# Optimization experiments

Hardware: AMD Instinct MI355X
Metric: run time of the kernel (lower is better)

Reference implementation:

```python
import jax, jax.numpy as jnp
import numpy as np

ND, NC = 100000, 20000
E_DD, E_DC, E_CD = 1600000, 800000, 800000
DDIM, CDIM, H, B = 256, 512, 128, 100000


def _lin_init(k, out_d, in_d):
    kw, kb = jax.random.split(k)
    s = 1.0 / np.sqrt(in_d)
    return (jax.random.uniform(kw, (out_d, in_d), jnp.float32, -s, s),
            jax.random.uniform(kb, (out_d,), jnp.float32, -s, s))


def setup_inputs() -> dict:
    key = jax.random.key(0)
    ks = jax.random.split(key, 32)
    inp = {
        'x_drug': jax.random.normal(ks[0], (ND, DDIM), jnp.float32),
        'x_cell': jax.random.normal(ks[1], (NC, CDIM), jnp.float32),
        'ei_dd_src': jax.random.randint(ks[2], (E_DD,), 0, ND),
        'ei_dd_dst': jax.random.randint(ks[3], (E_DD,), 0, ND),
        'ei_dc_src': jax.random.randint(ks[4], (E_DC,), 0, ND),
        'ei_dc_dst': jax.random.randint(ks[5], (E_DC,), 0, NC),
        'ei_cd_src': jax.random.randint(ks[6], (E_CD,), 0, NC),
        'ei_cd_dst': jax.random.randint(ks[7], (E_CD,), 0, ND),
        'q_da': jax.random.randint(ks[8], (B,), 0, ND),
        'q_db': jax.random.randint(ks[9], (B,), 0, ND),
        'q_c': jax.random.randint(ks[10], (B,), 0, NC),
    }
    # input projections
    inp['wd'], inp['bd'] = _lin_init(ks[11], H, DDIM)
    inp['wc'], inp['bc'] = _lin_init(ks[12], H, CDIM)
    # per-edge-type SAGEConv params: lin_l (W+b, on aggregated neighbors), lin_r (W only, on root)
    i = 13
    for name in ['dd1', 'cd1', 'dc1', 'dd2', 'cd2', 'dc2']:
        wl, bl = _lin_init(ks[i], H, H)
        wr, _ = _lin_init(ks[i + 1], H, H)
        inp[name + '_wl'], inp[name + '_bl'], inp[name + '_wr'] = wl, bl, wr
        i += 2
    # MLP head
    inp['m1_w'], inp['m1_b'] = _lin_init(ks[i], H, 3 * H)
    inp['m2_w'], inp['m2_b'] = _lin_init(ks[i + 1], 1, H)
    return inp


def _sage(x_src, x_dst, src, dst, wl, bl, wr):
    # SAGEConv: mean-aggregate neighbor (src) features onto dst, then lin_l + lin_r(root)
    n_dst = x_dst.shape[0]
    agg = jax.ops.segment_sum(x_src[src], dst, num_segments=n_dst)  # [n_dst, H]
    cnt = jax.ops.segment_sum(jnp.ones(src.shape, x_src.dtype), dst, num_segments=n_dst)
    mean = agg / jnp.maximum(cnt, 1.0)[:, None]
    return mean @ wl.T + bl + x_dst @ wr.T


def reference(x_drug, x_cell, wd, bd, wc, bc,
              dd1_wl, dd1_bl, dd1_wr, cd1_wl, cd1_bl, cd1_wr, dc1_wl, dc1_bl, dc1_wr,
              dd2_wl, dd2_bl, dd2_wr, cd2_wl, cd2_bl, cd2_wr, dc2_wl, dc2_bl, dc2_wr,
              m1_w, m1_b, m2_w, m2_b,
              ei_dd_src, ei_dd_dst, ei_dc_src, ei_dc_dst, ei_cd_src, ei_cd_dst,
              q_da, q_db, q_c):
    xd = x_drug @ wd.T + bd  # [ND, H]
    xc = x_cell @ wc.T + bc  # [NC, H]
    # layer 1 (to_hetero: sum contributions per dst node type, then relu)
    hd = jax.nn.relu(_sage(xd, xd, ei_dd_src, ei_dd_dst, dd1_wl, dd1_bl, dd1_wr)
                     + _sage(xc, xd, ei_cd_src, ei_cd_dst, cd1_wl, cd1_bl, cd1_wr))
    hc = jax.nn.relu(_sage(xd, xc, ei_dc_src, ei_dc_dst, dc1_wl, dc1_bl, dc1_wr))
    # layer 2 (no activation)
    od = (_sage(hd, hd, ei_dd_src, ei_dd_dst, dd2_wl, dd2_bl, dd2_wr)
          + _sage(hc, hd, ei_cd_src, ei_cd_dst, cd2_wl, cd2_bl, cd2_wr))
    oc = _sage(hd, hc, ei_dc_src, ei_dc_dst, dc2_wl, dc2_bl, dc2_wr)
    combined = jnp.concatenate([od[q_da], od[q_db], oc[q_c]], axis=-1)  # [B, 3H]
    h = jax.nn.relu(combined @ m1_w.T + m1_b)  # dropout is eval-mode identity
    return (h @ m2_w.T + m2_b)[:, 0]
```

## Files before the change

### kernel.cpp

```cpp
#include <hip/hip_runtime.h>
#include <hip/hip_fp16.h>

typedef _Float16 f16;
typedef f16 f16x8 __attribute__((ext_vector_type(8)));
typedef float f32x4 __attribute__((ext_vector_type(4)));

#define NDRUG 100000
#define NCELL 20000
#define EDD   1600000
#define EDC   800000
#define ECD   800000
#define NQ    100000
#define ETOT  (EDD + ECD + EDC)
#define NNODE 220000

#define NBD 782
#define NBC 313
#define NBTOT (NBD + NBC)
#define ECHUNK 8192
#define NBLK ((ETOT + ECHUNK - 1) / ECHUNK)
#define BCAP 8192
#define LCAP 6144

__device__ inline int bucket_of(int rdst) { return rdst < 200000 ? (rdst >> 8) : NBD + ((rdst - 200000) >> 6); }
__device__ inline int dl_of(int rdst)     { return rdst < 200000 ? (rdst & 255) : ((rdst - 200000) & 63); }


__global__ __launch_bounds__(256) void scatter_k(
    const int* __restrict__ dds, const int* __restrict__ ddd,
    const int* __restrict__ cds, const int* __restrict__ cdd,
    const int* __restrict__ dcs, const int* __restrict__ dcd,
    int* __restrict__ bucket_cur, unsigned* __restrict__ binned)
{
    __shared__ int lh[NBTOT];
    __shared__ int lbase[NBTOT];

    int tid = threadIdx.x;
    for (int i = tid; i < NBTOT; i += 256) lh[i] = 0;
    __syncthreads();

    int base = blockIdx.x * ECHUNK;
    int end = base + ECHUNK; if (end > ETOT) end = ETOT;

    for (int e = base + tid; e < end; e += 256) {
        int rdst;
        if (e < EDD) rdst = ddd[e];
        else if (e < EDD + ECD) rdst = 100000 + cdd[e - EDD];
        else rdst = 200000 + dcd[e - EDD - ECD];
        atomicAdd(&lh[bucket_of(rdst)], 1);
    }
    __syncthreads();

    for (int i = tid; i < NBTOT; i += 256) {
        int c = lh[i];
        lbase[i] = c ? atomicAdd(&bucket_cur[i], c) : 0;
        lh[i] = 0;
    }
    __syncthreads();

    for (int e = base + tid; e < end; e += 256) {
        int src, rdst;
        if (e < EDD) { src = dds[e]; rdst = ddd[e]; }
        else if (e < EDD + ECD) { int i2 = e - EDD; src = cds[i2]; rdst = 100000 + cdd[i2]; }
        else { int i2 = e - EDD - ECD; src = dcs[i2]; rdst = 200000 + dcd[i2]; }
        int b = bucket_of(rdst);
        int r = atomicAdd(&lh[b], 1);
        binned[lbase[b] + r] = ((unsigned)dl_of(rdst) << 17) | (unsigned)src;
    }
}


__global__ __launch_bounds__(256) void scan_pbase_k(const int* __restrict__ bucket_cur,
                                                    int* __restrict__ pbase, int* __restrict__ rowptr)
{
    __shared__ int seg[256];
    int tid = threadIdx.x;
    int mine[5], s = 0;
#pragma unroll
    for (int q = 0; q < 5; ++q) {
        int idx = tid * 5 + q;
        int t = 0;
        if (idx < NBTOT) {
            t = bucket_cur[idx] - idx * BCAP;
            t = t < 0 ? 0 : (t > LCAP ? LCAP : t);
        }
        mine[q] = t; s += t;
    }
    seg[tid] = s; __syncthreads();
    for (int o = 1; o < 256; o <<= 1) {
        int v = (tid >= o) ? seg[tid - o] : 0;
        __syncthreads();
        seg[tid] += v;
        __syncthreads();
    }
    int run = seg[tid] - s;
#pragma unroll
    for (int q = 0; q < 5; ++q) {
        int idx = tid * 5 + q;
        if (idx < NBTOT) pbase[idx] = run;
        run += mine[q];
    }
    if (tid == 255) { pbase[NBTOT] = seg[255]; rowptr[NNODE] = seg[255]; }
}


__global__ __launch_bounds__(256) void bucket_build_k(
    const unsigned* __restrict__ binned, const int* __restrict__ bucket_cur, const int* __restrict__ pbase,
    int* __restrict__ rowptr, int* __restrict__ packed)
{
    __shared__ int cnt[256];
    __shared__ int off[256];
    __shared__ int seg[256];
    __shared__ unsigned short lrank[LCAP];
    __shared__ unsigned srec[LCAP];

    int b = blockIdx.x, tid = threadIdx.x;
    int gbase = b * BCAP;
    int n = bucket_cur[b] - gbase;
    n = n < 0 ? 0 : (n > LCAP ? LCAP : n);
    int pb = pbase[b];

    cnt[tid] = 0;
    __syncthreads();
    for (int j = tid; j < n; j += 256) {
        unsigned r = binned[gbase + j];
        lrank[j] = (unsigned short)atomicAdd(&cnt[r >> 17], 1);
    }
    __syncthreads();
    int c = cnt[tid];
    seg[tid] = c; __syncthreads();
    for (int o = 1; o < 256; o <<= 1) {
        int v = (tid >= o) ? seg[tid - o] : 0;
        __syncthreads();
        seg[tid] += v;
        __syncthreads();
    }
    off[tid] = seg[tid] - c;
    __syncthreads();

    if (b < NBD) {
        int rdst = b * 256 + tid;
        if (rdst < 200000) rowptr[rdst] = pb + off[tid];
    } else {
        if (tid < 64) {
            int node = (b - NBD) * 64 + tid;
            if (node < NCELL) rowptr[200000 + node] = pb + off[tid];
        }
    }

    for (int j = tid; j < n; j += 256) {
        unsigned r = binned[gbase + j];
        int p = off[r >> 17] + lrank[j];
        srec[p] = r & 0x1FFFF;
    }
    __syncthreads();

    for (int p = tid; p < n; p += 256) packed[pb + p] = (int)srec[p];
}


__global__ __launch_bounds__(256) void cvt16_k(const float* __restrict__ xd, f16* __restrict__ xd16,
                                               const float* __restrict__ xc, f16* __restrict__ xc16)
{
    const long TD = (long)NDRUG * 256 / 8;
    const long TC = (long)NCELL * 512 / 8;
    long stride = (long)gridDim.x * 256;
    for (long t = (long)blockIdx.x * 256 + threadIdx.x; t < TD + TC; t += stride) {
        const float* src; f16* dst;
        long p;
        if (t < TD) { src = xd; dst = xd16; p = t; }
        else        { src = xc; dst = xc16; p = t - TD; }
        const float4* sp = (const float4*)(src + p * 8);
        float4 u = sp[0], v = sp[1];
        f16x8 h;
        h[0] = (f16)u.x; h[1] = (f16)u.y; h[2] = (f16)u.z; h[3] = (f16)u.w;
        h[4] = (f16)v.x; h[5] = (f16)v.y; h[6] = (f16)v.z; h[7] = (f16)v.w;
        *(f16x8*)(dst + p * 8) = h;
    }
}


__device__ inline void addv(float* acc, uint4 v)
{
    const __half2* h = (const __half2*)&v;
#pragma unroll
    for (int j = 0; j < 4; ++j) {
        float2 f = __half22float2(h[j]);
        acc[2 * j]     += f.x;
        acc[2 * j + 1] += f.y;
    }
}

__global__ __launch_bounds__(256) void agg_all_k(
    const __half* __restrict__ t_d, const __half* __restrict__ t_c,
    const int* __restrict__ rowptr, const int* __restrict__ packed,
    __half* __restrict__ m_a, __half* __restrict__ m_b, __half* __restrict__ m_c)
{
    int gid = blockIdx.x * 16 + (threadIdx.x >> 4);
    if (gid >= NNODE) return;
    int g = threadIdx.x & 15;

    const __half* tab; __half* out;
    if (gid < 100000)      { tab = t_d; out = m_a + (size_t)gid * 128; }
    else if (gid < 200000) { tab = t_c; out = m_b + (size_t)(gid - 100000) * 128; }
    else                   { tab = t_d; out = m_c + (size_t)(gid - 200000) * 128; }

    int s = rowptr[gid];
    int n = rowptr[gid + 1] - s;
    const int* list = packed + s;
    const __half* base = tab + (size_t)g * 8;

    float acc[8];
#pragma unroll
    for (int j = 0; j < 8; ++j) acc[j] = 0.f;

    int i = 0;
    for (; i + 3 < n; i += 4) {
        int s0 = list[i], s1 = list[i + 1], s2 = list[i + 2], s3 = list[i + 3];
        uint4 v0 = *(const uint4*)(base + (size_t)s0 * 128);
        uint4 v1 = *(const uint4*)(base + (size_t)s1 * 128);
        uint4 v2 = *(const uint4*)(base + (size_t)s2 * 128);
        uint4 v3 = *(const uint4*)(base + (size_t)s3 * 128);
        addv(acc, v0); addv(acc, v1); addv(acc, v2); addv(acc, v3);
    }
    for (; i < n; ++i) {
        uint4 v = *(const uint4*)(base + (size_t)list[i] * 128);
        addv(acc, v);
    }

    float inv = 1.f / fmaxf((float)n, 1.f);
    __half h[8];
#pragma unroll
    for (int j = 0; j < 8; ++j) h[j] = __float2half(acc[j] * inv);
    *(uint4*)(out + g * 8) = *(uint4*)h;
}


__global__ __launch_bounds__(256) void prep_k(
    const float* __restrict__ wd,     const float* __restrict__ wc,     const float* __restrict__ m1w,
    const float* __restrict__ dd1_wl, const float* __restrict__ cd1_wl, const float* __restrict__ dc1_wl,
    const float* __restrict__ dc1_wr, const float* __restrict__ dd1_wr, const float* __restrict__ cd1_wr,
    const float* __restrict__ dd1_bl, const float* __restrict__ cd1_bl,
    const float* __restrict__ dd2_wl, const float* __restrict__ cd2_wl, const float* __restrict__ dc2_wl,
    const float* __restrict__ dc2_wr, const float* __restrict__ dd2_wr, const float* __restrict__ cd2_wr,
    const float* __restrict__ dd2_bl, const float* __restrict__ cd2_bl,
    f16* __restrict__ wd16, f16* __restrict__ wc16, f16* __restrict__ m1w16,
    f16* __restrict__ dd1_wl16, f16* __restrict__ cd1_wl16, f16* __restrict__ dc1_wl16,
    f16* __restrict__ dc1_wr16, f16* __restrict__ wr1s16,
    f16* __restrict__ dd2_wl16, f16* __restrict__ cd2_wl16, f16* __restrict__ dc2_wl16,
    f16* __restrict__ dc2_wr16, f16* __restrict__ wr2s16,
    float* __restrict__ bsum1, float* __restrict__ bsum2,
    int* __restrict__ bucket_cur)
{
    int i = blockIdx.x * 256 + threadIdx.x;
    if (i < 128 * 256) wd16[i] = (f16)wd[i];
    if (i < 128 * 512) wc16[i] = (f16)wc[i];
    if (i < 128 * 384) m1w16[i] = (f16)m1w[i];
    if (i < 128 * 128) {
        dd1_wl16[i] = (f16)dd1_wl[i];
        cd1_wl16[i] = (f16)cd1_wl[i];
        dc1_wl16[i] = (f16)dc1_wl[i];
        dc1_wr16[i] = (f16)dc1_wr[i];
        wr1s16[i]   = (f16)(dd1_wr[i] + cd1_wr[i]);
        dd2_wl16[i] = (f16)dd2_wl[i];
        cd2_wl16[i] = (f16)cd2_wl[i];
        dc2_wl16[i] = (f16)dc2_wl[i];
        dc2_wr16[i] = (f16)dc2_wr[i];
        wr2s16[i]   = (f16)(dd2_wr[i] + cd2_wr[i]);
    }
    if (i < 128) {
        bsum1[i] = dd1_bl[i] + cd1_bl[i];
        bsum2[i] = dd2_bl[i] + cd2_bl[i];
    }
    if (i < NBTOT) bucket_cur[i] = i * BCAP;
}


template<typename AT, int MODE>
__global__ __launch_bounds__(256) void mgemm_k(
    const AT* A00, const int* I00, const f16* W00, int K00, int S00,
    const AT* A01, const int* I01, const f16* W01, int K01, int S01,
    const AT* A02, const int* I02, const f16* W02, int K02, int S02,
    const float* bias0, f16* Ch0, int M0,
    const AT* A10, const int* I10, const f16* W10, int K10, int S10,
    const AT* A11, const int* I11, const f16* W11, int K11, int S11,
    const AT* A12, const int* I12, const f16* W12, int K12, int S12,
    const float* bias1, f16* Ch1, int M1,
    int split,
    const float* m2w, const float* m2b, float* Cf)
{
    __shared__ f16 As[128][72];
    __shared__ f16 Ws[128][72];

    const int tid = threadIdx.x;
    const int w  = tid >> 6;
    const int l  = tid & 63;
    const int lc = l & 15;
    const int lq = l >> 4;
    const int sr = tid >> 1;
    const int sk = (tid & 1) * 32;

    const bool j1 = (int)blockIdx.x >= split;
    const int mb = ((int)blockIdx.x - (j1 ? split : 0)) * 128;
    const AT*  Aseg[3] = { j1 ? A10 : A00, j1 ? A11 : A01, j1 ? A12 : A02 };
    const int* Iseg[3] = { j1 ? I10 : I00, j1 ? I11 : I01, j1 ? I12 : I02 };
    const f16* Wseg[3] = { j1 ? W10 : W00, j1 ? W11 : W01, j1 ? W12 : W02 };
    const int  Kseg[3] = { j1 ? K10 : K00, j1 ? K11 : K01, j1 ? K12 : K02 };
    const int  Sseg[3] = { j1 ? S10 : S00, j1 ? S11 : S01, j1 ? S12 : S02 };
    const float* bias = j1 ? bias1 : bias0;
    f16* Ch = j1 ? Ch1 : Ch0;
    const int M = j1 ? M1 : M0;

    f32x4 acc[2][8];
#pragma unroll
    for (int mi = 0; mi < 2; ++mi)
#pragma unroll
        for (int j = 0; j < 8; ++j) acc[mi][j] = (f32x4){0.f, 0.f, 0.f, 0.f};

    for (int s = 0; s < 3; ++s) {
        const AT* A = Aseg[s];
        if (!A) continue;
        const int* idx = Iseg[s];
        const f16* W = Wseg[s];
        const int K = Kseg[s], S = Sseg[s];

        int m = mb + sr; if (m >= M) m = M - 1;
        const AT*  arow = A + (size_t)(idx ? idx[m] : m) * (size_t)K;
        const f16* wrow = W + (size_t)sr * (size_t)S;

        for (int kt = 0; kt < K; kt += 64) {
            if constexpr (sizeof(AT) == 2) {
                const uint4* ap = (const uint4*)(arow + kt + sk);
                uint4 a0 = ap[0], a1 = ap[1], a2 = ap[2], a3 = ap[3];
                *(uint4*)&As[sr][sk]      = a0;
                *(uint4*)&As[sr][sk + 8]  = a1;
                *(uint4*)&As[sr][sk + 16] = a2;
                *(uint4*)&As[sr][sk + 24] = a3;
            } else {
                const float4* ap = (const float4*)(arow + kt + sk);
#pragma unroll
                for (int i = 0; i < 4; ++i) {
                    float4 u = ap[2 * i], v = ap[2 * i + 1];
                    f16x8 h;
                    h[0] = (f16)u.x; h[1] = (f16)u.y; h[2] = (f16)u.z; h[3] = (f16)u.w;
                    h[4] = (f16)v.x; h[5] = (f16)v.y; h[6] = (f16)v.z; h[7] = (f16)v.w;
                    *(f16x8*)&As[sr][sk + 8 * i] = h;
                }
            }
            {
                const uint4* wp = (const uint4*)(wrow + kt + sk);
                uint4 w0 = wp[0], w1 = wp[1], w2 = wp[2], w3 = wp[3];
                *(uint4*)&Ws[sr][sk]      = w0;
                *(uint4*)&Ws[sr][sk + 8]  = w1;
                *(uint4*)&Ws[sr][sk + 16] = w2;
                *(uint4*)&Ws[sr][sk + 24] = w3;
            }
            __syncthreads();

#pragma unroll
            for (int ks = 0; ks < 64; ks += 32) {
                f16x8 a0 = *(const f16x8*)&As[32 * w + lc][ks + 8 * lq];
                f16x8 a1 = *(const f16x8*)&As[32 * w + 16 + lc][ks + 8 * lq];
#pragma unroll
                for (int j = 0; j < 8; ++j) {
                    f16x8 b = *(const f16x8*)&Ws[16 * j + lc][ks + 8 * lq];
                    acc[0][j] = __builtin_amdgcn_mfma_f32_16x16x32_f16(a0, b, acc[0][j], 0, 0, 0);
                    acc[1][j] = __builtin_amdgcn_mfma_f32_16x16x32_f16(a1, b, acc[1][j], 0, 0, 0);
                }
            }
            __syncthreads();
        }
    }

    if (MODE == 2) {
        float part[2][4];
#pragma unroll
        for (int mi = 0; mi < 2; ++mi)
#pragma unroll
            for (int r = 0; r < 4; ++r) part[mi][r] = 0.f;
#pragma unroll
        for (int j = 0; j < 8; ++j) {
            float bj = bias[16 * j + lc];
            float wv = m2w[16 * j + lc];
#pragma unroll
            for (int mi = 0; mi < 2; ++mi)
#pragma unroll
                for (int r = 0; r < 4; ++r) {
                    float v = acc[mi][j][r] + bj;
                    v = v > 0.f ? v : 0.f;
                    part[mi][r] = fmaf(v, wv, part[mi][r]);
                }
        }
#pragma unroll
        for (int mi = 0; mi < 2; ++mi)
#pragma unroll
            for (int r = 0; r < 4; ++r) {
                float p = part[mi][r];
#pragma unroll
                for (int o = 1; o < 16; o <<= 1) p += __shfl_xor(p, o, 16);
                if (lc == 0) {
                    int row = mb + 32 * w + 16 * mi + 4 * lq + r;
                    if (row < M) Cf[row] = p + m2b[0];
                }
            }
    } else {
#pragma unroll
        for (int j = 0; j < 8; ++j) {
            float bj = bias[16 * j + lc];
#pragma unroll
            for (int mi = 0; mi < 2; ++mi)
#pragma unroll
                for (int r = 0; r < 4; ++r) {
                    float v = acc[mi][j][r] + bj;
                    if (MODE == 1) v = v > 0.f ? v : 0.f;
                    int row = mb + 32 * w + 16 * mi + 4 * lq + r;
                    if (row < M) Ch[(size_t)row * 128 + 16 * j + lc] = (f16)v;
                }
        }
    }
}


extern "C" void kernel_launch(void* const* d_in, const int* in_sizes, int n_in,
                              void* d_out, int out_size, void* d_ws, size_t ws_size,
                              hipStream_t stream)
{
    const float* x_drug = (const float*)d_in[0];
    const float* x_cell = (const float*)d_in[1];
    const int* ei_dd_src = (const int*)d_in[2];
    const int* ei_dd_dst = (const int*)d_in[3];
    const int* ei_dc_src = (const int*)d_in[4];
    const int* ei_dc_dst = (const int*)d_in[5];
    const int* ei_cd_src = (const int*)d_in[6];
    const int* ei_cd_dst = (const int*)d_in[7];
    const int* q_da = (const int*)d_in[8];
    const int* q_db = (const int*)d_in[9];
    const int* q_c  = (const int*)d_in[10];
    const float* wd = (const float*)d_in[11];
    const float* bd = (const float*)d_in[12];
    const float* wc = (const float*)d_in[13];
    const float* bc = (const float*)d_in[14];
    const float* dd1_wl = (const float*)d_in[15]; const float* dd1_bl = (const float*)d_in[16]; const float* dd1_wr = (const float*)d_in[17];
    const float* cd1_wl = (const float*)d_in[18]; const float* cd1_bl = (const float*)d_in[19]; const float* cd1_wr = (const float*)d_in[20];
    const float* dc1_wl = (const float*)d_in[21]; const float* dc1_bl = (const float*)d_in[22]; const float* dc1_wr = (const float*)d_in[23];
    const float* dd2_wl = (const float*)d_in[24]; const float* dd2_bl = (const float*)d_in[25]; const float* dd2_wr = (const float*)d_in[26];
    const float* cd2_wl = (const float*)d_in[27]; const float* cd2_bl = (const float*)d_in[28]; const float* cd2_wr = (const float*)d_in[29];
    const float* dc2_wl = (const float*)d_in[30]; const float* dc2_bl = (const float*)d_in[31]; const float* dc2_wr = (const float*)d_in[32];
    const float* m1_w = (const float*)d_in[33]; const float* m1_b = (const float*)d_in[34];
    const float* m2_w = (const float*)d_in[35]; const float* m2_b = (const float*)d_in[36];
    float* out = (float*)d_out;

    char* wsp = (char*)d_ws;
    size_t off = 0;
    auto alloc = [&](size_t bytes) -> void* {
        void* p = wsp + off;
        off += (bytes + 255) & ~(size_t)255;
        return p;
    };

    f16* xd32_16 = (f16*)alloc((size_t)NDRUG * 256 * 2);
    f16* xc32_16 = (f16*)alloc((size_t)NCELL * 512 * 2);

    __half* xd_h     = (__half*)alloc((size_t)NDRUG * 128 * 2);
    __half* xc_h     = (__half*)alloc((size_t)NCELL * 128 * 2);
    __half* hd_h     = (__half*)alloc((size_t)NDRUG * 128 * 2);
    __half* hc_h     = (__half*)alloc((size_t)NCELL * 128 * 2);
    __half* mean_a_h = (__half*)alloc((size_t)NDRUG * 128 * 2);
    __half* mean_b_h = (__half*)alloc((size_t)NDRUG * 128 * 2);
    __half* mean_c_h = (__half*)alloc((size_t)NCELL * 128 * 2);
    __half* od_h     = (__half*)alloc((size_t)NDRUG * 128 * 2);
    __half* oc_h     = (__half*)alloc((size_t)NCELL * 128 * 2);

    f16* wd16     = (f16*)alloc(128 * 256 * 2);
    f16* wc16     = (f16*)alloc(128 * 512 * 2);
    f16* m1w16    = (f16*)alloc(128 * 384 * 2);
    f16* dd1_wl16 = (f16*)alloc(128 * 128 * 2);
    f16* cd1_wl16 = (f16*)alloc(128 * 128 * 2);
    f16* dc1_wl16 = (f16*)alloc(128 * 128 * 2);
    f16* dc1_wr16 = (f16*)alloc(128 * 128 * 2);
    f16* wr1s16   = (f16*)alloc(128 * 128 * 2);
    f16* dd2_wl16 = (f16*)alloc(128 * 128 * 2);
    f16* cd2_wl16 = (f16*)alloc(128 * 128 * 2);
    f16* dc2_wl16 = (f16*)alloc(128 * 128 * 2);
    f16* dc2_wr16 = (f16*)alloc(128 * 128 * 2);
    f16* wr2s16   = (f16*)alloc(128 * 128 * 2);
    float* bsum1  = (float*)alloc(128 * 4);
    float* bsum2  = (float*)alloc(128 * 4);

    int* bucket_cur  = (int*)alloc((size_t)NBTOT * 4);
    int* pbase       = (int*)alloc((size_t)(NBTOT + 1) * 4);
    int* rowptr      = (int*)alloc((size_t)(NNODE + 1) * 4);
    int* packed      = (int*)alloc((size_t)ETOT * 4);
    unsigned* binned = (unsigned*)alloc((size_t)NBTOT * BCAP * 4);

    prep_k<<<256, 256, 0, stream>>>(
        wd, wc, m1_w,
        dd1_wl, cd1_wl, dc1_wl, dc1_wr, dd1_wr, cd1_wr, dd1_bl, cd1_bl,
        dd2_wl, cd2_wl, dc2_wl, dc2_wr, dd2_wr, cd2_wr, dd2_bl, cd2_bl,
        wd16, wc16, m1w16,
        dd1_wl16, cd1_wl16, dc1_wl16, dc1_wr16, wr1s16,
        dd2_wl16, cd2_wl16, dc2_wl16, dc2_wr16, wr2s16,
        bsum1, bsum2, bucket_cur);

    cvt16_k<<<4096, 256, 0, stream>>>(x_drug, xd32_16, x_cell, xc32_16);

    scatter_k<<<NBLK, 256, 0, stream>>>(ei_dd_src, ei_dd_dst, ei_cd_src, ei_cd_dst,
                                        ei_dc_src, ei_dc_dst, bucket_cur, binned);
    scan_pbase_k<<<1, 256, 0, stream>>>(bucket_cur, pbase, rowptr);
    bucket_build_k<<<NBTOT, 256, 0, stream>>>(binned, bucket_cur, pbase, rowptr, packed);

    const f16*   fnull = nullptr;
    const float* f32null = nullptr;
    const int*   inull = nullptr;
    const int GD = (NDRUG + 127) / 128;
    const int GC = (NCELL + 127) / 128;
    const int GQ = (NQ + 127) / 128;

    mgemm_k<f16, 0><<<GD + GC, 256, 0, stream>>>(
        xc32_16, inull, wc16, 512, 512,
        fnull, inull, fnull, 0, 0,
        fnull, inull, fnull, 0, 0,
        bc, (f16*)xc_h, NCELL,
        xd32_16, inull, wd16, 256, 256,
        fnull, inull, fnull, 0, 0,
        fnull, inull, fnull, 0, 0,
        bd, (f16*)xd_h, NDRUG,
        GC, f32null, f32null, nullptr);

    const int AGG_GRID = (NNODE + 15) / 16;

    agg_all_k<<<AGG_GRID, 256, 0, stream>>>(xd_h, xc_h, rowptr, packed,
                                            mean_a_h, mean_b_h, mean_c_h);

    mgemm_k<f16, 1><<<GD + GC, 256, 0, stream>>>(
        (const f16*)mean_c_h, inull, dc1_wl16, 128, 128,
        (const f16*)xc_h,     inull, dc1_wr16, 128, 128,
        fnull,                inull, fnull,    0, 0,
        dc1_bl, (f16*)hc_h, NCELL,
        (const f16*)mean_a_h, inull, dd1_wl16, 128, 128,
        (const f16*)mean_b_h, inull, cd1_wl16, 128, 128,
        (const f16*)xd_h,     inull, wr1s16,   128, 128,
        bsum1, (f16*)hd_h, NDRUG,
        GC, f32null, f32null, nullptr);

    agg_all_k<<<AGG_GRID, 256, 0, stream>>>(hd_h, hc_h, rowptr, packed,
                                            mean_a_h, mean_b_h, mean_c_h);

    mgemm_k<f16, 0><<<GD + GC, 256, 0, stream>>>(
        (const f16*)mean_c_h, inull, dc2_wl16, 128, 128,
        (const f16*)hc_h,     inull, dc2_wr16, 128, 128,
        fnull,                inull, fnull,    0, 0,
        dc2_bl, (f16*)oc_h, NCELL,
        (const f16*)mean_a_h, inull, dd2_wl16, 128, 128,
        (const f16*)mean_b_h, inull, cd2_wl16, 128, 128,
        (const f16*)hd_h,     inull, wr2s16,   128, 128,
        bsum2, (f16*)od_h, NDRUG,
        GC, f32null, f32null, nullptr);

    mgemm_k<f16, 2><<<GQ, 256, 0, stream>>>(
        (const f16*)od_h, q_da, m1w16,       128, 384,
        (const f16*)od_h, q_db, m1w16 + 128, 128, 384,
        (const f16*)oc_h, q_c,  m1w16 + 256, 128, 384,
        m1_b, nullptr, NQ,
        fnull, inull, fnull, 0, 0,
        fnull, inull, fnull, 0, 0,
        fnull, inull, fnull, 0, 0,
        f32null, nullptr, 0,
        GQ, m2_w, m2_b, out);
}
```

Measured before the change: 482.2 us.

## Merge graph-build stages with conversion and projection kernels, drop compacted CSR

The fp32-to-fp16 conversion now runs as extra blocks inside the edge scatter kernel. The bucket sort and the input projection GEMM share one launch through a shared-memory union. The prefix scan over buckets and the separate packed array are removed: sorted edges are written back in place into the padded binned buffer, and aggregation reads a per-node count array instead of rowptr[i+1]. This cuts three launches, one global scan and one copy of the edge list, at the cost of larger shared-memory footprints and more heterogeneous blocks per kernel.

Measured after the change: 467.3 us. -3.1%, faster.

```diff
diff --git a/kernel.cpp b/kernel.cpp
--- a/kernel.cpp
+++ b/kernel.cpp
@@ -21,161 +21,276 @@
 #define NBLK ((ETOT + ECHUNK - 1) / ECHUNK)
 #define BCAP 8192
 #define LCAP 6144
+#define CVTG 2048
+#define GC_PROJ 157
+#define GD_PROJ 782
 
 __device__ inline int bucket_of(int rdst) { return rdst < 200000 ? (rdst >> 8) : NBD + ((rdst - 200000) >> 6); }
 __device__ inline int dl_of(int rdst)     { return rdst < 200000 ? (rdst & 255) : ((rdst - 200000) & 63); }
 
 
-__global__ __launch_bounds__(256) void scatter_k(
+struct GemmSh { f16 As[128][72]; f16 Ws[128][72]; };
+struct BktSh {
+    int cnt[256]; int off[256]; int seg[256];
+    unsigned short lrank[LCAP];
+    unsigned srec[LCAP];
+};
+union ShU { GemmSh g; BktSh b; };
+
+
+template<typename AT, int MODE>
+__device__ __forceinline__ void gemm_core(
+    f16 (*As)[72], f16 (*Ws)[72], int mb,
+    const AT* A0, const int* I0, const f16* W0, int K0, int S0,
+    const AT* A1, const int* I1, const f16* W1, int K1, int S1,
+    const AT* A2, const int* I2, const f16* W2, int K2, int S2,
+    const float* bias, f16* Ch, int M,
+    const float* m2w, const float* m2b, float* Cf)
+{
+    const int tid = threadIdx.x;
+    const int w  = tid >> 6;
+    const int l  = tid & 63;
+    const int lc = l & 15;
+    const int lq = l >> 4;
+    const int sr = tid >> 1;
+    const int sk = (tid & 1) * 32;
+
+    f32x4 acc[2][8];
+#pragma unroll
+    for (int mi = 0; mi < 2; ++mi)
+#pragma unroll
+        for (int j = 0; j < 8; ++j) acc[mi][j] = (f32x4){0.f, 0.f, 0.f, 0.f};
+
+    const AT*  Aseg[3] = {A0, A1, A2};
+    const int* Iseg[3] = {I0, I1, I2};
+    const f16* Wseg[3] = {W0, W1, W2};
+    const int  Kseg[3] = {K0, K1, K2};
+    const int  Sseg[3] = {S0, S1, S2};
+
+    for (int s = 0; s < 3; ++s) {
+        const AT* A = Aseg[s];
+        if (!A) continue;
+        const int* idx = Iseg[s];
+        const f16* W = Wseg[s];
+        const int K = Kseg[s], S = Sseg[s];
+
+        int m = mb + sr; if (m >= M) m = M - 1;
+        const AT*  arow = A + (size_t)(idx ? idx[m] : m) * (size_t)K;
+        const f16* wrow = W + (size_t)sr * (size_t)S;
+
+        for (int kt = 0; kt < K; kt += 64) {
+            {
+                const uint4* ap = (const uint4*)(arow + kt + sk);
+                uint4 a0 = ap[0], a1 = ap[1], a2 = ap[2], a3 = ap[3];
+                *(uint4*)&As[sr][sk]      = a0;
+                *(uint4*)&As[sr][sk + 8]  = a1;
+                *(uint4*)&As[sr][sk + 16] = a2;
+                *(uint4*)&As[sr][sk + 24] = a3;
+            }
+            {
+                const uint4* wp = (const uint4*)(wrow + kt + sk);
+                uint4 w0 = wp[0], w1 = wp[1], w2 = wp[2], w3 = wp[3];
+                *(uint4*)&Ws[sr][sk]      = w0;
+                *(uint4*)&Ws[sr][sk + 8]  = w1;
+                *(uint4*)&Ws[sr][sk + 16] = w2;
+                *(uint4*)&Ws[sr][sk + 24] = w3;
+            }
+            __syncthreads();
+
+#pragma unroll
+            for (int ks = 0; ks < 64; ks += 32) {
+                f16x8 a0 = *(const f16x8*)&As[32 * w + lc][ks + 8 * lq];
+                f16x8 a1 = *(const f16x8*)&As[32 * w + 16 + lc][ks + 8 * lq];
+#pragma unroll
+                for (int j = 0; j < 8; ++j) {
+                    f16x8 b = *(const f16x8*)&Ws[16 * j + lc][ks + 8 * lq];
+                    acc[0][j] = __builtin_amdgcn_mfma_f32_16x16x32_f16(a0, b, acc[0][j], 0, 0, 0);
+                    acc[1][j] = __builtin_amdgcn_mfma_f32_16x16x32_f16(a1, b, acc[1][j], 0, 0, 0);
+                }
+            }
+            __syncthreads();
+        }
+    }
+
+    if (MODE == 2) {
+        float part[2][4];
+#pragma unroll
+        for (int mi = 0; mi < 2; ++mi)
+#pragma unroll
+            for (int r = 0; r < 4; ++r) part[mi][r] = 0.f;
+#pragma unroll
+        for (int j = 0; j < 8; ++j) {
+            float bj = bias[16 * j + lc];
+            float wv = m2w[16 * j + lc];
+#pragma unroll
+            for (int mi = 0; mi < 2; ++mi)
+#pragma unroll
+                for (int r = 0; r < 4; ++r) {
+                    float v = acc[mi][j][r] + bj;
+                    v = v > 0.f ? v : 0.f;
+                    part[mi][r] = fmaf(v, wv, part[mi][r]);
+                }
+        }
+#pragma unroll
+        for (int mi = 0; mi < 2; ++mi)
+#pragma unroll
+            for (int r = 0; r < 4; ++r) {
+                float p = part[mi][r];
+#pragma unroll
+                for (int o = 1; o < 16; o <<= 1) p += __shfl_xor(p, o, 16);
+                if (lc == 0) {
+                    int row = mb + 32 * w + 16 * mi + 4 * lq + r;
+                    if (row < M) Cf[row] = p + m2b[0];
+                }
+            }
+    } else {
+#pragma unroll
+        for (int j = 0; j < 8; ++j) {
+            float bj = bias[16 * j + lc];
+#pragma unroll
+            for (int mi = 0; mi < 2; ++mi)
+#pragma unroll
+                for (int r = 0; r < 4; ++r) {
+                    float v = acc[mi][j][r] + bj;
+                    if (MODE == 1) v = v > 0.f ? v : 0.f;
+                    int row = mb + 32 * w + 16 * mi + 4 * lq + r;
+                    if (row < M) Ch[(size_t)row * 128 + 16 * j + lc] = (f16)v;
+                }
+        }
+    }
+}
+
+
+__global__ __launch_bounds__(256) void scatter_cvt_k(
     const int* __restrict__ dds, const int* __restrict__ ddd,
     const int* __restrict__ cds, const int* __restrict__ cdd,
     const int* __restrict__ dcs, const int* __restrict__ dcd,
-    int* __restrict__ bucket_cur, unsigned* __restrict__ binned)
+    int* __restrict__ bucket_cur, unsigned* __restrict__ binned,
+    const float* __restrict__ xd, f16* __restrict__ xd16,
+    const float* __restrict__ xc, f16* __restrict__ xc16)
 {
     __shared__ int lh[NBTOT];
     __shared__ int lbase[NBTOT];
-
     int tid = threadIdx.x;
-    for (int i = tid; i < NBTOT; i += 256) lh[i] = 0;
-    __syncthreads();
-
-    int base = blockIdx.x * ECHUNK;
-    int end = base + ECHUNK; if (end > ETOT) end = ETOT;
-
-    for (int e = base + tid; e < end; e += 256) {
-        int rdst;
-        if (e < EDD) rdst = ddd[e];
-        else if (e < EDD + ECD) rdst = 100000 + cdd[e - EDD];
-        else rdst = 200000 + dcd[e - EDD - ECD];
-        atomicAdd(&lh[bucket_of(rdst)], 1);
-    }
-    __syncthreads();
-
-    for (int i = tid; i < NBTOT; i += 256) {
-        int c = lh[i];
-        lbase[i] = c ? atomicAdd(&bucket_cur[i], c) : 0;
-        lh[i] = 0;
-    }
-    __syncthreads();
-
-    for (int e = base + tid; e < end; e += 256) {
-        int src, rdst;
-        if (e < EDD) { src = dds[e]; rdst = ddd[e]; }
-        else if (e < EDD + ECD) { int i2 = e - EDD; src = cds[i2]; rdst = 100000 + cdd[i2]; }
-        else { int i2 = e - EDD - ECD; src = dcs[i2]; rdst = 200000 + dcd[i2]; }
-        int b = bucket_of(rdst);
-        int r = atomicAdd(&lh[b], 1);
-        binned[lbase[b] + r] = ((unsigned)dl_of(rdst) << 17) | (unsigned)src;
-    }
-}
-
-
-__global__ __launch_bounds__(256) void scan_pbase_k(const int* __restrict__ bucket_cur,
-                                                    int* __restrict__ pbase, int* __restrict__ rowptr)
-{
-    __shared__ int seg[256];
+
+    if ((int)blockIdx.x < NBLK) {
+        for (int i = tid; i < NBTOT; i += 256) lh[i] = 0;
+        __syncthreads();
+
+        int base = blockIdx.x * ECHUNK;
+        int end = base + ECHUNK; if (end > ETOT) end = ETOT;
+
+        for (int e = base + tid; e < end; e += 256) {
+            int rdst;
+            if (e < EDD) rdst = ddd[e];
+            else if (e < EDD + ECD) rdst = 100000 + cdd[e - EDD];
+            else rdst = 200000 + dcd[e - EDD - ECD];
+            atomicAdd(&lh[bucket_of(rdst)], 1);
+        }
+        __syncthreads();
+
+        for (int i = tid; i < NBTOT; i += 256) {
+            int c = lh[i];
+            lbase[i] = c ? atomicAdd(&bucket_cur[i], c) : 0;
+            lh[i] = 0;
+        }
+        __syncthreads();
+
+        for (int e = base + tid; e < end; e += 256) {
+            int src, rdst;
+            if (e < EDD) { src = dds[e]; rdst = ddd[e]; }
+            else if (e < EDD + ECD) { int i2 = e - EDD; src = cds[i2]; rdst = 100000 + cdd[i2]; }
+            else { int i2 = e - EDD - ECD; src = dcs[i2]; rdst = 200000 + dcd[i2]; }
+            int b = bucket_of(rdst);
+            int r = atomicAdd(&lh[b], 1);
+            binned[lbase[b] + r] = ((unsigned)dl_of(rdst) << 17) | (unsigned)src;
+        }
+    } else {
+        const long TD = (long)NDRUG * 256 / 8;
+        const long TC = (long)NCELL * 512 / 8;
+        long stride = (long)CVTG * 256;
+        for (long t = (long)((int)blockIdx.x - NBLK) * 256 + tid; t < TD + TC; t += stride) {
+            const float* src; f16* dst; long p;
+            if (t < TD) { src = xd; dst = xd16; p = t; }
+            else        { src = xc; dst = xc16; p = t - TD; }
+            const float4* sp = (const float4*)(src + p * 8);
+            float4 u = sp[0], v = sp[1];
+            f16x8 h;
+            h[0] = (f16)u.x; h[1] = (f16)u.y; h[2] = (f16)u.z; h[3] = (f16)u.w;
+            h[4] = (f16)v.x; h[5] = (f16)v.y; h[6] = (f16)v.z; h[7] = (f16)v.w;
+            *(f16x8*)(dst + p * 8) = h;
+        }
+    }
+}
+
+
+__global__ __launch_bounds__(256) void bucket_proj_k(
+    unsigned* __restrict__ binned, const int* __restrict__ bucket_cur,
+    int* __restrict__ rowptr, int* __restrict__ cnt_arr,
+    const f16* __restrict__ xc32_16, const f16* __restrict__ wc16, const float* __restrict__ bc, f16* __restrict__ xc_h,
+    const f16* __restrict__ xd32_16, const f16* __restrict__ wd16, const float* __restrict__ bd, f16* __restrict__ xd_h)
+{
+    __shared__ ShU sh;
     int tid = threadIdx.x;
-    int mine[5], s = 0;
-#pragma unroll
-    for (int q = 0; q < 5; ++q) {
-        int idx = tid * 5 + q;
-        int t = 0;
-        if (idx < NBTOT) {
-            t = bucket_cur[idx] - idx * BCAP;
-            t = t < 0 ? 0 : (t > LCAP ? LCAP : t);
-        }
-        mine[q] = t; s += t;
-    }
-    seg[tid] = s; __syncthreads();
-    for (int o = 1; o < 256; o <<= 1) {
-        int v = (tid >= o) ? seg[tid - o] : 0;
-        __syncthreads();
-        seg[tid] += v;
-        __syncthreads();
-    }
-    int run = seg[tid] - s;
-#pragma unroll
-    for (int q = 0; q < 5; ++q) {
-        int idx = tid * 5 + q;
-        if (idx < NBTOT) pbase[idx] = run;
-        run += mine[q];
-    }
-    if (tid == 255) { pbase[NBTOT] = seg[255]; rowptr[NNODE] = seg[255]; }
-}
-
-
-__global__ __launch_bounds__(256) void bucket_build_k(
-    const unsigned* __restrict__ binned, const int* __restrict__ bucket_cur, const int* __restrict__ pbase,
-    int* __restrict__ rowptr, int* __restrict__ packed)
-{
-    __shared__ int cnt[256];
-    __shared__ int off[256];
-    __shared__ int seg[256];
-    __shared__ unsigned short lrank[LCAP];
-    __shared__ unsigned srec[LCAP];
-
-    int b = blockIdx.x, tid = threadIdx.x;
-    int gbase = b * BCAP;
-    int n = bucket_cur[b] - gbase;
-    n = n < 0 ? 0 : (n > LCAP ? LCAP : n);
-    int pb = pbase[b];
-
-    cnt[tid] = 0;
-    __syncthreads();
-    for (int j = tid; j < n; j += 256) {
-        unsigned r = binned[gbase + j];
-        lrank[j] = (unsigned short)atomicAdd(&cnt[r >> 17], 1);
-    }
-    __syncthreads();
-    int c = cnt[tid];
-    seg[tid] = c; __syncthreads();
-    for (int o = 1; o < 256; o <<= 1) {
-        int v = (tid >= o) ? seg[tid - o] : 0;
-        __syncthreads();
-        seg[tid] += v;
-        __syncthreads();
-    }
-    off[tid] = seg[tid] - c;
-    __syncthreads();
-
-    if (b < NBD) {
-        int rdst = b * 256 + tid;
-        if (rdst < 200000) rowptr[rdst] = pb + off[tid];
+
+    if ((int)blockIdx.x < NBTOT) {
+        int b = blockIdx.x;
+        int gbase = b * BCAP;
+        int n = bucket_cur[b] - gbase;
+        n = n < 0 ? 0 : (n > LCAP ? LCAP : n);
+
+        sh.b.cnt[tid] = 0;
+        __syncthreads();
+        for (int j = tid; j < n; j += 256) {
+            unsigned r = binned[gbase + j];
+            sh.b.lrank[j] = (unsigned short)atomicAdd(&sh.b.cnt[r >> 17], 1);
+        }
+        __syncthreads();
+        int c = sh.b.cnt[tid];
+        sh.b.seg[tid] = c; __syncthreads();
+        for (int o = 1; o < 256; o <<= 1) {
+            int v = (tid >= o) ? sh.b.seg[tid - o] : 0;
+            __syncthreads();
+            sh.b.seg[tid] += v;
+            __syncthreads();
+        }
+        sh.b.off[tid] = sh.b.seg[tid] - c;
+        __syncthreads();
+
+        if (b < NBD) {
+            int rdst = b * 256 + tid;
+            if (rdst < 200000) { rowptr[rdst] = gbase + sh.b.off[tid]; cnt_arr[rdst] = c; }
+        } else {
+            if (tid < 64) {
+                int node = (b - NBD) * 64 + tid;
+                if (node < NCELL) { rowptr[200000 + node] = gbase + sh.b.off[tid]; cnt_arr[200000 + node] = c; }
+            }
+        }
+
+        for (int j = tid; j < n; j += 256) {
+            unsigned r = binned[gbase + j];
+            int p = sh.b.off[r >> 17] + sh.b.lrank[j];
+            sh.b.srec[p] = r & 0x1FFFF;
+        }
+        __syncthreads();
+
+        for (int p = tid; p < n; p += 256) binned[gbase + p] = sh.b.srec[p];
     } else {
-        if (tid < 64) {
-            int node = (b - NBD) * 64 + tid;
-            if (node < NCELL) rowptr[200000 + node] = pb + off[tid];
-        }
-    }
-
-    for (int j = tid; j < n; j += 256) {
-        unsigned r = binned[gbase + j];
-        int p = off[r >> 17] + lrank[j];
-        srec[p] = r & 0x1FFFF;
-    }
-    __syncthreads();
-
-    for (int p = tid; p < n; p += 256) packed[pb + p] = (int)srec[p];
-}
-
-
-__global__ __launch_bounds__(256) void cvt16_k(const float* __restrict__ xd, f16* __restrict__ xd16,
-                                               const float* __restrict__ xc, f16* __restrict__ xc16)
-{
-    const long TD = (long)NDRUG * 256 / 8;
-    const long TC = (long)NCELL * 512 / 8;
-    long stride = (long)gridDim.x * 256;
-    for (long t = (long)blockIdx.x * 256 + threadIdx.x; t < TD + TC; t += stride) {
-        const float* src; f16* dst;
-        long p;
-        if (t < TD) { src = xd; dst = xd16; p = t; }
-        else        { src = xc; dst = xc16; p = t - TD; }
-        const float4* sp = (const float4*)(src + p * 8);
-        float4 u = sp[0], v = sp[1];
-        f16x8 h;
-        h[0] = (f16)u.x; h[1] = (f16)u.y; h[2] = (f16)u.z; h[3] = (f16)u.w;
-        h[4] = (f16)v.x; h[5] = (f16)v.y; h[6] = (f16)v.z; h[7] = (f16)v.w;
-        *(f16x8*)(dst + p * 8) = h;
+        int bid = (int)blockIdx.x - NBTOT;
+        const f16* fn = nullptr; const int* in_ = nullptr;
+        if (bid < GC_PROJ) {
+            gemm_core<f16, 0>(sh.g.As, sh.g.Ws, bid * 128,
+                xc32_16, in_, wc16, 512, 512,
+                fn, in_, fn, 0, 0,
+                fn, in_, fn, 0, 0,
+                bc, xc_h, NCELL, nullptr, nullptr, nullptr);
+        } else {
+            gemm_core<f16, 0>(sh.g.As, sh.g.Ws, (bid - GC_PROJ) * 128,
+                xd32_16, in_, wd16, 256, 256,
+                fn, in_, fn, 0, 0,
+                fn, in_, fn, 0, 0,
+                bd, xd_h, NDRUG, nullptr, nullptr, nullptr);
+        }
     }
 }
 
@@ -193,7 +308,8 @@
 
 __global__ __launch_bounds__(256) void agg_all_k(
     const __half* __restrict__ t_d, const __half* __restrict__ t_c,
-    const int* __restrict__ rowptr, const int* __restrict__ packed,
+    const int* __restrict__ rowptr, const int* __restrict__ cnt_arr,
+    const unsigned* __restrict__ packed,
     __half* __restrict__ m_a, __half* __restrict__ m_b, __half* __restrict__ m_c)
 {
     int gid = blockIdx.x * 16 + (threadIdx.x >> 4);
@@ -206,8 +322,8 @@
     else                   { tab = t_d; out = m_c + (size_t)(gid - 200000) * 128; }
 
     int s = rowptr[gid];
-    int n = rowptr[gid + 1] - s;
-    const int* list = packed + s;
+    int n = cnt_arr[gid];
+    const unsigned* list = packed + s;
     const __half* base = tab + (size_t)g * 8;
 
     float acc[8];
@@ -216,7 +332,7 @@
 
     int i = 0;
     for (; i + 3 < n; i += 4) {
-        int s0 = list[i], s1 = list[i + 1], s2 = list[i + 2], s3 = list[i + 3];
+        unsigned s0 = list[i], s1 = list[i + 1], s2 = list[i + 2], s3 = list[i + 3];
         uint4 v0 = *(const uint4*)(base + (size_t)s0 * 128);
         uint4 v1 = *(const uint4*)(base + (size_t)s1 * 128);
         uint4 v2 = *(const uint4*)(base + (size_t)s2 * 128);
@@ -291,133 +407,14 @@
 {
     __shared__ f16 As[128][72];
     __shared__ f16 Ws[128][72];
-
-    const int tid = threadIdx.x;
-    const int w  = tid >> 6;
-    const int l  = tid & 63;
-    const int lc = l & 15;
-    const int lq = l >> 4;
-    const int sr = tid >> 1;
-    const int sk = (tid & 1) * 32;
-
     const bool j1 = (int)blockIdx.x >= split;
     const int mb = ((int)blockIdx.x - (j1 ? split : 0)) * 128;
-    const AT*  Aseg[3] = { j1 ? A10 : A00, j1 ? A11 : A01, j1 ? A12 : A02 };
-    const int* Iseg[3] = { j1 ? I10 : I00, j1 ? I11 : I01, j1 ? I12 : I02 };
-    const f16* Wseg[3] = { j1 ? W10 : W00, j1 ? W11 : W01, j1 ? W12 : W02 };
-    const int  Kseg[3] = { j1 ? K10 : K00, j1 ? K11 : K01, j1 ? K12 : K02 };
-    const int  Sseg[3] = { j1 ? S10 : S00, j1 ? S11 : S01, j1 ? S12 : S02 };
-    const float* bias = j1 ? bias1 : bias0;
-    f16* Ch = j1 ? Ch1 : Ch0;
-    const int M = j1 ? M1 : M0;
-
-    f32x4 acc[2][8];
-#pragma unroll
-    for (int mi = 0; mi < 2; ++mi)
-#pragma unroll
-        for (int j = 0; j < 8; ++j) acc[mi][j] = (f32x4){0.f, 0.f, 0.f, 0.f};
-
-    for (int s = 0; s < 3; ++s) {
-        const AT* A = Aseg[s];
-        if (!A) continue;
-        const int* idx = Iseg[s];
-        const f16* W = Wseg[s];
-        const int K = Kseg[s], S = Sseg[s];
-
-        int m = mb + sr; if (m >= M) m = M - 1;
-        const AT*  arow = A + (size_t)(idx ? idx[m] : m) * (size_t)K;
-        const f16* wrow = W + (size_t)sr * (size_t)S;
-
-        for (int kt = 0; kt < K; kt += 64) {
-            if constexpr (sizeof(AT) == 2) {
-                const uint4* ap = (const uint4*)(arow + kt + sk);
-                uint4 a0 = ap[0], a1 = ap[1], a2 = ap[2], a3 = ap[3];
-                *(uint4*)&As[sr][sk]      = a0;
-                *(uint4*)&As[sr][sk + 8]  = a1;
-                *(uint4*)&As[sr][sk + 16] = a2;
-                *(uint4*)&As[sr][sk + 24] = a3;
-            } else {
-                const float4* ap = (const float4*)(arow + kt + sk);
-#pragma unroll
-                for (int i = 0; i < 4; ++i) {
-                    float4 u = ap[2 * i], v = ap[2 * i + 1];
-                    f16x8 h;
-                    h[0] = (f16)u.x; h[1] = (f16)u.y; h[2] = (f16)u.z; h[3] = (f16)u.w;
-                    h[4] = (f16)v.x; h[5] = (f16)v.y; h[6] = (f16)v.z; h[7] = (f16)v.w;
-                    *(f16x8*)&As[sr][sk + 8 * i] = h;
-                }
-            }
-            {
-                const uint4* wp = (const uint4*)(wrow + kt + sk);
-                uint4 w0 = wp[0], w1 = wp[1], w2 = wp[2], w3 = wp[3];
-                *(uint4*)&Ws[sr][sk]      = w0;
-                *(uint4*)&Ws[sr][sk + 8]  = w1;
-                *(uint4*)&Ws[sr][sk + 16] = w2;
-                *(uint4*)&Ws[sr][sk + 24] = w3;
-            }
-            __syncthreads();
-
-#pragma unroll
-            for (int ks = 0; ks < 64; ks += 32) {
-                f16x8 a0 = *(const f16x8*)&As[32 * w + lc][ks + 8 * lq];
-                f16x8 a1 = *(const f16x8*)&As[32 * w + 16 + lc][ks + 8 * lq];
-#pragma unroll
-                for (int j = 0; j < 8; ++j) {
-                    f16x8 b = *(const f16x8*)&Ws[16 * j + lc][ks + 8 * lq];
-                    acc[0][j] = __builtin_amdgcn_mfma_f32_16x16x32_f16(a0, b, acc[0][j], 0, 0, 0);
-                    acc[1][j] = __builtin_amdgcn_mfma_f32_16x16x32_f16(a1, b, acc[1][j], 0, 0, 0);
-                }
-            }
-            __syncthreads();
-        }
-    }
-
-    if (MODE == 2) {
-        float part[2][4];
-#pragma unroll
-        for (int mi = 0; mi < 2; ++mi)
-#pragma unroll
-            for (int r = 0; r < 4; ++r) part[mi][r] = 0.f;
-#pragma unroll
-        for (int j = 0; j < 8; ++j) {
-            float bj = bias[16 * j + lc];
-            float wv = m2w[16 * j + lc];
-#pragma unroll
-            for (int mi = 0; mi < 2; ++mi)
-#pragma unroll
-                for (int r = 0; r < 4; ++r) {
-                    float v = acc[mi][j][r] + bj;
-                    v = v > 0.f ? v : 0.f;
-                    part[mi][r] = fmaf(v, wv, part[mi][r]);
-                }
-        }
-#pragma unroll
-        for (int mi = 0; mi < 2; ++mi)
-#pragma unroll
-            for (int r = 0; r < 4; ++r) {
-                float p = part[mi][r];
-#pragma unroll
-                for (int o = 1; o < 16; o <<= 1) p += __shfl_xor(p, o, 16);
-                if (lc == 0) {
-                    int row = mb + 32 * w + 16 * mi + 4 * lq + r;
-                    if (row < M) Cf[row] = p + m2b[0];
-                }
-            }
-    } else {
-#pragma unroll
-        for (int j = 0; j < 8; ++j) {
-            float bj = bias[16 * j + lc];
-#pragma unroll
-            for (int mi = 0; mi < 2; ++mi)
-#pragma unroll
-                for (int r = 0; r < 4; ++r) {
-                    float v = acc[mi][j][r] + bj;
-                    if (MODE == 1) v = v > 0.f ? v : 0.f;
-                    int row = mb + 32 * w + 16 * mi + 4 * lq + r;
-                    if (row < M) Ch[(size_t)row * 128 + 16 * j + lc] = (f16)v;
-                }
-        }
-    }
+    if (!j1)
+        gemm_core<AT, MODE>(As, Ws, mb, A00, I00, W00, K00, S00, A01, I01, W01, K01, S01,
+                            A02, I02, W02, K02, S02, bias0, Ch0, M0, m2w, m2b, Cf);
+    else
+        gemm_core<AT, MODE>(As, Ws, mb, A10, I10, W10, K10, S10, A11, I11, W11, K11, S11,
+                            A12, I12, W12, K12, S12, bias1, Ch1, M1, m2w, m2b, Cf);
 }
 
 
@@ -488,9 +485,8 @@
     float* bsum2  = (float*)alloc(128 * 4);
 
     int* bucket_cur  = (int*)alloc((size_t)NBTOT * 4);
-    int* pbase       = (int*)alloc((size_t)(NBTOT + 1) * 4);
-    int* rowptr      = (int*)alloc((size_t)(NNODE + 1) * 4);
-    int* packed      = (int*)alloc((size_t)ETOT * 4);
+    int* rowptr      = (int*)alloc((size_t)NNODE * 4);
+    int* cnt_arr     = (int*)alloc((size_t)NNODE * 4);
     unsigned* binned = (unsigned*)alloc((size_t)NBTOT * BCAP * 4);
 
     prep_k<<<256, 256, 0, stream>>>(
@@ -502,34 +498,25 @@
         dd2_wl16, cd2_wl16, dc2_wl16, dc2_wr16, wr2s16,
         bsum1, bsum2, bucket_cur);
 
-    cvt16_k<<<4096, 256, 0, stream>>>(x_drug, xd32_16, x_cell, xc32_16);
-
-    scatter_k<<<NBLK, 256, 0, stream>>>(ei_dd_src, ei_dd_dst, ei_cd_src, ei_cd_dst,
-                                        ei_dc_src, ei_dc_dst, bucket_cur, binned);
-    scan_pbase_k<<<1, 256, 0, stream>>>(bucket_cur, pbase, rowptr);
-    bucket_build_k<<<NBTOT, 256, 0, stream>>>(binned, bucket_cur, pbase, rowptr, packed);
+    scatter_cvt_k<<<NBLK + CVTG, 256, 0, stream>>>(
+        ei_dd_src, ei_dd_dst, ei_cd_src, ei_cd_dst, ei_dc_src, ei_dc_dst,
+        bucket_cur, binned, x_drug, xd32_16, x_cell, xc32_16);
+
+    bucket_proj_k<<<NBTOT + GC_PROJ + GD_PROJ, 256, 0, stream>>>(
+        binned, bucket_cur, rowptr, cnt_arr,
+        xc32_16, wc16, bc, (f16*)xc_h,
+        xd32_16, wd16, bd, (f16*)xd_h);
 
     const f16*   fnull = nullptr;
     const float* f32null = nullptr;
     const int*   inull = nullptr;
-    const int GD = (NDRUG + 127) / 128;
-    const int GC = (NCELL + 127) / 128;
+    const int GD = GD_PROJ;
+    const int GC = GC_PROJ;
     const int GQ = (NQ + 127) / 128;
 
-    mgemm_k<f16, 0><<<GD + GC, 256, 0, stream>>>(
-        xc32_16, inull, wc16, 512, 512,
-        fnull, inull, fnull, 0, 0,
-        fnull, inull, fnull, 0, 0,
-        bc, (f16*)xc_h, NCELL,
-        xd32_16, inull, wd16, 256, 256,
-        fnull, inull, fnull, 0, 0,
-        fnull, inull, fnull, 0, 0,
-        bd, (f16*)xd_h, NDRUG,
-        GC, f32null, f32null, nullptr);
-
     const int AGG_GRID = (NNODE + 15) / 16;
 
-    agg_all_k<<<AGG_GRID, 256, 0, stream>>>(xd_h, xc_h, rowptr, packed,
+    agg_all_k<<<AGG_GRID, 256, 0, stream>>>(xd_h, xc_h, rowptr, cnt_arr, binned,
                                             mean_a_h, mean_b_h, mean_c_h);
 
     mgemm_k<f16, 1><<<GD + GC, 256, 0, stream>>>(
@@ -543,7 +530,7 @@
         bsum1, (f16*)hd_h, NDRUG,
         GC, f32null, f32null, nullptr);
 
-    agg_all_k<<<AGG_GRID, 256, 0, stream>>>(hd_h, hc_h, rowptr, packed,
+    agg_all_k<<<AGG_GRID, 256, 0, stream>>>(hd_h, hc_h, rowptr, cnt_arr, binned,
                                             mean_a_h, mean_b_h, mean_c_h);
 
     mgemm_k<f16, 0><<<GD + GC, 256, 0, stream>>>(
```
